# Kernel optimization log

Hardware: AMD Instinct MI355X
Metric: run time of the kernel (lower is better)

## Reference

```python
import jax, jax.numpy as jnp
import numpy as np

B, T, D, A = 32, 4096, 512, 64


def setup_inputs() -> dict:
    key = jax.random.key(0)
    k_x, k_m, k_w1, k_b1, k_w2 = jax.random.split(key, 5)
    x = jax.random.normal(k_x, (B, T, D), dtype=jnp.float32)
    mask = jax.random.randint(k_m, (B, T), 0, 2) > 0
    mask = mask.at[:, 0].set(True)  # guarantee >=1 valid step per row
    # params of attention MLP: Linear(D->A) with bias, Linear(A->1) no bias
    W1 = jax.random.normal(k_w1, (A, D), dtype=jnp.float32) / np.sqrt(D)
    b1 = jax.random.normal(k_b1, (A,), dtype=jnp.float32) * 0.01
    w2 = jax.random.normal(k_w2, (A,), dtype=jnp.float32) / np.sqrt(A)
    return {"x": x, "mask": mask, "W1": W1, "b1": b1, "w2": w2}


def reference(x, mask, W1, b1, w2):
    h = jnp.tanh(jnp.einsum('btd,ad->bta', x, W1) + b1)
    scores = jnp.einsum('bta,a->bt', h, w2)
    scores = jnp.where(mask, scores, -jnp.inf)
    weights = jax.nn.softmax(scores, axis=-1)          # (B, T)
    context = jnp.einsum('bt,btd->bd', weights, x)     # (B, D)
    return context, weights
```

## Files before the change

### kernel.cpp

```cpp
#include <hip/hip_runtime.h>
#include <math.h>

#define NB 32
#define NT 4096
#define ND 512
#define NA 64
#define ND4 (ND / 4)
#define RPB 128
#define NBLK (NB * NT / RPB)
#define NPW (NT / RPB)

typedef __attribute__((ext_vector_type(8))) short short8;
typedef __attribute__((ext_vector_type(4))) float f32x4;

__device__ __forceinline__ uint cvtpk(float f0, float f1) {
    uint r;
    asm("v_cvt_pk_bf16_f32 %0, %1, %2" : "=v"(r) : "v"(f0), "v"(f1));
    return r;
}
__device__ __forceinline__ void split2(float f0, float f1, uint& hw, uint& lw) {
    hw = cvtpk(f0, f1);
    float r0 = f0 - __uint_as_float(hw << 16);
    float r1 = f1 - __uint_as_float(hw & 0xffff0000u);
    lw = cvtpk(r0, r1);
}
__device__ __forceinline__ void split8(float4 a, float4 b, short8& hi, short8& lo) {
    union U { short8 s; uint u[4]; } H, L;
    split2(a.x, a.y, H.u[0], L.u[0]);
    split2(a.z, a.w, H.u[1], L.u[1]);
    split2(b.x, b.y, H.u[2], L.u[2]);
    split2(b.z, b.w, H.u[3], L.u[3]);
    hi = H.s; lo = L.s;
}

__device__ __forceinline__ float fast_tanh(float z) {
    z = fminf(fmaxf(z, -15.f), 15.f);
    float t = __expf(2.f * z);
    return (t - 1.f) * __builtin_amdgcn_rcpf(t + 1.f);
}

__global__ __launch_bounds__(256) void k_prep(
    const float* __restrict__ W1, short8* __restrict__ whi, short8* __restrict__ wlo)
{
    int t = blockIdx.x * 256 + threadIdx.x;
    int l  = t & 63;
    int nt = (t >> 6) & 3;
    int ks = t >> 8;
    int a  = nt * 16 + (l & 15);
    int kb = ks * 32 + (l >> 4) * 8;
    const float* p = W1 + a * ND + kb;
    float4 u = *(const float4*)p;
    float4 v = *(const float4*)(p + 4);
    short8 hi, lo;
    split8(u, v, hi, lo);
    whi[t] = hi;
    wlo[t] = lo;
}

__global__ __launch_bounds__(256, 4) void k_fused(
    const float* __restrict__ x, const int* __restrict__ mask,
    const short8* __restrict__ whi, const short8* __restrict__ wlo,
    const float* __restrict__ b1, const float* __restrict__ w2,
    float* __restrict__ scores, float* __restrict__ pctx, float* __restrict__ pml)
{
    __shared__ float ctxl[4][ND];
    __shared__ float wmx[4], wlx[4];

    const int tid = threadIdx.x;
    const int wv  = tid >> 6;
    const int l   = tid & 63;
    const int lr  = l & 15;
    const int lq  = l >> 4;
    const size_t row0 = (size_t)blockIdx.x * RPB + (size_t)wv * 32;

    const float4* __restrict__ x4 = reinterpret_cast<const float4*>(x);
    const float* xb = x + (row0 + lr) * ND + lq * 8;

    float w2v[4], b1v[4];
#pragma unroll
    for (int nt = 0; nt < 4; ++nt) {
        w2v[nt] = w2[nt * 16 + lr];
        b1v[nt] = b1[nt * 16 + lr];
    }

    f32x4 acc[2][4];
#pragma unroll
    for (int mt = 0; mt < 2; ++mt)
#pragma unroll
        for (int nt = 0; nt < 4; ++nt) acc[mt][nt] = (f32x4)0.f;

    for (int ks = 0; ks < 16; ++ks) {
        short8 ahi[2], alo[2];
#pragma unroll
        for (int mt = 0; mt < 2; ++mt) {
            const float* p = xb + mt * 16 * ND + ks * 32;
            float4 u = *(const float4*)p;
            float4 v = *(const float4*)(p + 4);
            split8(u, v, ahi[mt], alo[mt]);
        }
#pragma unroll
        for (int nt = 0; nt < 4; ++nt) {
            short8 bh = whi[(ks * 4 + nt) * 64 + l];
            short8 bl = wlo[(ks * 4 + nt) * 64 + l];
#pragma unroll
            for (int mt = 0; mt < 2; ++mt) {
                acc[mt][nt] = __builtin_amdgcn_mfma_f32_16x16x32_bf16(ahi[mt], bh, acc[mt][nt], 0, 0, 0);
                acc[mt][nt] = __builtin_amdgcn_mfma_f32_16x16x32_bf16(ahi[mt], bl, acc[mt][nt], 0, 0, 0);
                acc[mt][nt] = __builtin_amdgcn_mfma_f32_16x16x32_bf16(alo[mt], bh, acc[mt][nt], 0, 0, 0);
            }
        }
    }

    float sval[2][4];
#pragma unroll
    for (int mt = 0; mt < 2; ++mt) {
#pragma unroll
        for (int rg = 0; rg < 4; ++rg) {
            float s = 0.f;
#pragma unroll
            for (int nt = 0; nt < 4; ++nt)
                s += w2v[nt] * fast_tanh(acc[mt][nt][rg] + b1v[nt]);
            s += __shfl_xor(s, 1);
            s += __shfl_xor(s, 2);
            s += __shfl_xor(s, 4);
            s += __shfl_xor(s, 8);
            int ridx = mt * 16 + lq * 4 + rg;
            bool valid = (mask[row0 + ridx] != 0);
            float sm = valid ? s : -INFINITY;
            if (lr == 0) scores[row0 + ridx] = sm;
            sval[mt][rg] = sm;
        }
    }

    float wm = -INFINITY;
#pragma unroll
    for (int mt = 0; mt < 2; ++mt)
#pragma unroll
        for (int rg = 0; rg < 4; ++rg) wm = fmaxf(wm, sval[mt][rg]);
    wm = fmaxf(wm, __shfl_xor(wm, 16));
    wm = fmaxf(wm, __shfl_xor(wm, 32));
    float wm_eff = (wm == -INFINITY) ? 0.f : wm;
    float ev[2][4];
#pragma unroll
    for (int mt = 0; mt < 2; ++mt)
#pragma unroll
        for (int rg = 0; rg < 4; ++rg) ev[mt][rg] = __expf(sval[mt][rg] - wm_eff);
    float wl = (ev[0][0] + ev[0][1]) + (ev[0][2] + ev[0][3])
             + (ev[1][0] + ev[1][1]) + (ev[1][2] + ev[1][3]);
    wl += __shfl_xor(wl, 16);
    wl += __shfl_xor(wl, 32);
    if (l == 0) { wmx[wv] = wm; wlx[wv] = wl; }

    float4 ca = {0.f, 0.f, 0.f, 0.f}, cb = {0.f, 0.f, 0.f, 0.f};
#pragma unroll
    for (int t = 0; t < 32; ++t) {
        float e = __shfl(ev[t >> 4][t & 3], ((t >> 2) & 3) * 16);
        float4 xa = x4[(row0 + t) * ND4 + l];
        float4 xv = x4[(row0 + t) * ND4 + 64 + l];
        ca.x = fmaf(e, xa.x, ca.x);
        ca.y = fmaf(e, xa.y, ca.y);
        ca.z = fmaf(e, xa.z, ca.z);
        ca.w = fmaf(e, xa.w, ca.w);
        cb.x = fmaf(e, xv.x, cb.x);
        cb.y = fmaf(e, xv.y, cb.y);
        cb.z = fmaf(e, xv.z, cb.z);
        cb.w = fmaf(e, xv.w, cb.w);
    }

    __syncthreads();
    float mb = fmaxf(fmaxf(wmx[0], wmx[1]), fmaxf(wmx[2], wmx[3]));
    float mb_eff = (mb == -INFINITY) ? 0.f : mb;
    float sw = __expf(wm - mb_eff);
    float4 sa = {ca.x * sw, ca.y * sw, ca.z * sw, ca.w * sw};
    float4 sb = {cb.x * sw, cb.y * sw, cb.z * sw, cb.w * sw};
    *(float4*)&ctxl[wv][4 * l]       = sa;
    *(float4*)&ctxl[wv][256 + 4 * l] = sb;
    __syncthreads();

    float s0 = (ctxl[0][tid] + ctxl[1][tid]) + (ctxl[2][tid] + ctxl[3][tid]);
    int t2 = tid + 256;
    float s1 = (ctxl[0][t2] + ctxl[1][t2]) + (ctxl[2][t2] + ctxl[3][t2]);
    pctx[(size_t)blockIdx.x * ND + tid] = s0;
    pctx[(size_t)blockIdx.x * ND + t2]  = s1;
    if (tid == 0) {
        float lt = wlx[0] * __expf(wmx[0] - mb_eff) + wlx[1] * __expf(wmx[1] - mb_eff)
                 + wlx[2] * __expf(wmx[2] - mb_eff) + wlx[3] * __expf(wmx[3] - mb_eff);
        pml[blockIdx.x * 2]     = mb;
        pml[blockIdx.x * 2 + 1] = lt;
    }
}

__global__ __launch_bounds__(256) void k_merge(
    const float* __restrict__ pctx, const float* __restrict__ pml,
    float* __restrict__ ctx, float* __restrict__ mbden)
{
    int b = blockIdx.x, tid = threadIdx.x;
    float m_b = -INFINITY;
    for (int i = 0; i < NPW; ++i) m_b = fmaxf(m_b, pml[(b * NPW + i) * 2]);
    float denom = 0.f;
    for (int i = 0; i < NPW; ++i) {
        float mi = pml[(b * NPW + i) * 2];
        float li = pml[(b * NPW + i) * 2 + 1];
        denom += li * expf(mi - m_b);
    }
    float inv = 1.f / denom;
    int d0 = 2 * tid;
    float a0 = 0.f, a1 = 0.f;
    for (int i = 0; i < NPW; ++i) {
        float s = expf(pml[(b * NPW + i) * 2] - m_b);
        a0 = fmaf(pctx[(size_t)(b * NPW + i) * ND + d0],     s, a0);
        a1 = fmaf(pctx[(size_t)(b * NPW + i) * ND + d0 + 1], s, a1);
    }
    ctx[(size_t)b * ND + d0]     = a0 * inv;
    ctx[(size_t)b * ND + d0 + 1] = a1 * inv;
    if (tid == 0) {
        mbden[b * 2]     = m_b;
        mbden[b * 2 + 1] = denom;
    }
}

__global__ __launch_bounds__(256) void k_weights(
    const float* __restrict__ scores, const float* __restrict__ mbden,
    float* __restrict__ weights)
{
    int i = blockIdx.x * 256 + threadIdx.x;
    int b = i >> 12;
    float m  = mbden[b * 2];
    float dn = mbden[b * 2 + 1];
    weights[i] = expf(scores[i] - m) / dn;
}

extern "C" void kernel_launch(void* const* d_in, const int* in_sizes, int n_in,
                              void* d_out, int out_size, void* d_ws, size_t ws_size,
                              hipStream_t stream)
{
    const float* x    = (const float*)d_in[0];
    const int*   mask = (const int*)d_in[1];
    const float* W1   = (const float*)d_in[2];
    const float* b1   = (const float*)d_in[3];
    const float* w2   = (const float*)d_in[4];

    float* ctx     = (float*)d_out;
    float* weights = (float*)d_out + NB * ND;

    float* ws      = (float*)d_ws;
    float* scores  = ws;
    float* pctx    = ws + NB * NT;
    float* pml     = pctx + (size_t)NBLK * ND;
    float* mbden   = pml + NBLK * 2;
    short8* whi    = (short8*)(mbden + NB * 2);
    short8* wlo    = whi + 16 * 4 * 64;

    k_prep<<<16, 256, 0, stream>>>(W1, whi, wlo);
    k_fused<<<NBLK, 256, 0, stream>>>(x, mask, whi, wlo, b1, w2,
                                      scores, pctx, pml);
    k_merge<<<NB, 256, 0, stream>>>(pctx, pml, ctx, mbden);
    k_weights<<<NB * NT / 256, 256, 0, stream>>>(scores, mbden, weights);
}
```

Baseline: 110.0 us.

## Drop softmax max-subtraction and accumulate context using raw exponentiated scores

Drops the running-max stabilisation from the softmax. The tanh-bounded scores are exponentiated directly, so per-block partial contexts and denominators can be plain sums. This removes the per-wave max reduction, the rescale exps and the max bookkeeping in the merge and weights kernels. The weights kernel becomes a single multiply by a precomputed inverse denominator. It also interleaves the context accumulation into each 16-row score tile. The risk is exp overflow or lost precision if sum|w2| were large, since correctness now relies on scores being bounded by the w2 magnitude.

Result: slower. 206.4 us (+87.6%).

```diff
diff --git a/kernel.cpp b/kernel.cpp
--- a/kernel.cpp
+++ b/kernel.cpp
@@ -61,10 +61,10 @@
     const float* __restrict__ x, const int* __restrict__ mask,
     const short8* __restrict__ whi, const short8* __restrict__ wlo,
     const float* __restrict__ b1, const float* __restrict__ w2,
-    float* __restrict__ scores, float* __restrict__ pctx, float* __restrict__ pml)
+    float* __restrict__ escore, float* __restrict__ pctx, float* __restrict__ pden)
 {
     __shared__ float ctxl[4][ND];
-    __shared__ float wmx[4], wlx[4];
+    __shared__ float wlx[4];
 
     const int tid = threadIdx.x;
     const int wv  = tid >> 6;
@@ -111,7 +111,8 @@
         }
     }
 
-    float sval[2][4];
+    float ev[2][4];
+    float4 ca = {0.f, 0.f, 0.f, 0.f}, cb = {0.f, 0.f, 0.f, 0.f};
 #pragma unroll
     for (int mt = 0; mt < 2; ++mt) {
 #pragma unroll
@@ -126,55 +127,35 @@
             s += __shfl_xor(s, 8);
             int ridx = mt * 16 + lq * 4 + rg;
             bool valid = (mask[row0 + ridx] != 0);
-            float sm = valid ? s : -INFINITY;
-            if (lr == 0) scores[row0 + ridx] = sm;
-            sval[mt][rg] = sm;
-        }
-    }
-
-    float wm = -INFINITY;
-#pragma unroll
-    for (int mt = 0; mt < 2; ++mt)
-#pragma unroll
-        for (int rg = 0; rg < 4; ++rg) wm = fmaxf(wm, sval[mt][rg]);
-    wm = fmaxf(wm, __shfl_xor(wm, 16));
-    wm = fmaxf(wm, __shfl_xor(wm, 32));
-    float wm_eff = (wm == -INFINITY) ? 0.f : wm;
-    float ev[2][4];
-#pragma unroll
-    for (int mt = 0; mt < 2; ++mt)
-#pragma unroll
-        for (int rg = 0; rg < 4; ++rg) ev[mt][rg] = __expf(sval[mt][rg] - wm_eff);
+            float e = valid ? __expf(s) : 0.f;
+            if (lr == 0) escore[row0 + ridx] = e;
+            ev[mt][rg] = e;
+        }
+#pragma unroll
+        for (int t = 0; t < 16; ++t) {
+            float e = __shfl(ev[mt][t & 3], ((t >> 2) & 3) * 16);
+            size_t r = row0 + mt * 16 + t;
+            float4 xa = x4[r * ND4 + l];
+            float4 xv = x4[r * ND4 + 64 + l];
+            ca.x = fmaf(e, xa.x, ca.x);
+            ca.y = fmaf(e, xa.y, ca.y);
+            ca.z = fmaf(e, xa.z, ca.z);
+            ca.w = fmaf(e, xa.w, ca.w);
+            cb.x = fmaf(e, xv.x, cb.x);
+            cb.y = fmaf(e, xv.y, cb.y);
+            cb.z = fmaf(e, xv.z, cb.z);
+            cb.w = fmaf(e, xv.w, cb.w);
+        }
+    }
+
     float wl = (ev[0][0] + ev[0][1]) + (ev[0][2] + ev[0][3])
              + (ev[1][0] + ev[1][1]) + (ev[1][2] + ev[1][3]);
     wl += __shfl_xor(wl, 16);
     wl += __shfl_xor(wl, 32);
-    if (l == 0) { wmx[wv] = wm; wlx[wv] = wl; }
-
-    float4 ca = {0.f, 0.f, 0.f, 0.f}, cb = {0.f, 0.f, 0.f, 0.f};
-#pragma unroll
-    for (int t = 0; t < 32; ++t) {
-        float e = __shfl(ev[t >> 4][t & 3], ((t >> 2) & 3) * 16);
-        float4 xa = x4[(row0 + t) * ND4 + l];
-        float4 xv = x4[(row0 + t) * ND4 + 64 + l];
-        ca.x = fmaf(e, xa.x, ca.x);
-        ca.y = fmaf(e, xa.y, ca.y);
-        ca.z = fmaf(e, xa.z, ca.z);
-        ca.w = fmaf(e, xa.w, ca.w);
-        cb.x = fmaf(e, xv.x, cb.x);
-        cb.y = fmaf(e, xv.y, cb.y);
-        cb.z = fmaf(e, xv.z, cb.z);
-        cb.w = fmaf(e, xv.w, cb.w);
-    }
-
-    __syncthreads();
-    float mb = fmaxf(fmaxf(wmx[0], wmx[1]), fmaxf(wmx[2], wmx[3]));
-    float mb_eff = (mb == -INFINITY) ? 0.f : mb;
-    float sw = __expf(wm - mb_eff);
-    float4 sa = {ca.x * sw, ca.y * sw, ca.z * sw, ca.w * sw};
-    float4 sb = {cb.x * sw, cb.y * sw, cb.z * sw, cb.w * sw};
-    *(float4*)&ctxl[wv][4 * l]       = sa;
-    *(float4*)&ctxl[wv][256 + 4 * l] = sb;
+    if (l == 0) wlx[wv] = wl;
+
+    *(float4*)&ctxl[wv][4 * l]       = ca;
+    *(float4*)&ctxl[wv][256 + 4 * l] = cb;
     __syncthreads();
 
     float s0 = (ctxl[0][tid] + ctxl[1][tid]) + (ctxl[2][tid] + ctxl[3][tid]);
@@ -182,52 +163,36 @@
     float s1 = (ctxl[0][t2] + ctxl[1][t2]) + (ctxl[2][t2] + ctxl[3][t2]);
     pctx[(size_t)blockIdx.x * ND + tid] = s0;
     pctx[(size_t)blockIdx.x * ND + t2]  = s1;
-    if (tid == 0) {
-        float lt = wlx[0] * __expf(wmx[0] - mb_eff) + wlx[1] * __expf(wmx[1] - mb_eff)
-                 + wlx[2] * __expf(wmx[2] - mb_eff) + wlx[3] * __expf(wmx[3] - mb_eff);
-        pml[blockIdx.x * 2]     = mb;
-        pml[blockIdx.x * 2 + 1] = lt;
-    }
+    if (tid == 0)
+        pden[blockIdx.x] = (wlx[0] + wlx[1]) + (wlx[2] + wlx[3]);
 }
 
 __global__ __launch_bounds__(256) void k_merge(
-    const float* __restrict__ pctx, const float* __restrict__ pml,
-    float* __restrict__ ctx, float* __restrict__ mbden)
+    const float* __restrict__ pctx, const float* __restrict__ pden,
+    float* __restrict__ ctx, float* __restrict__ invden)
 {
     int b = blockIdx.x, tid = threadIdx.x;
-    float m_b = -INFINITY;
-    for (int i = 0; i < NPW; ++i) m_b = fmaxf(m_b, pml[(b * NPW + i) * 2]);
     float denom = 0.f;
-    for (int i = 0; i < NPW; ++i) {
-        float mi = pml[(b * NPW + i) * 2];
-        float li = pml[(b * NPW + i) * 2 + 1];
-        denom += li * expf(mi - m_b);
-    }
+    for (int i = 0; i < NPW; ++i) denom += pden[b * NPW + i];
     float inv = 1.f / denom;
     int d0 = 2 * tid;
     float a0 = 0.f, a1 = 0.f;
     for (int i = 0; i < NPW; ++i) {
-        float s = expf(pml[(b * NPW + i) * 2] - m_b);
-        a0 = fmaf(pctx[(size_t)(b * NPW + i) * ND + d0],     s, a0);
-        a1 = fmaf(pctx[(size_t)(b * NPW + i) * ND + d0 + 1], s, a1);
+        a0 += pctx[(size_t)(b * NPW + i) * ND + d0];
+        a1 += pctx[(size_t)(b * NPW + i) * ND + d0 + 1];
     }
     ctx[(size_t)b * ND + d0]     = a0 * inv;
     ctx[(size_t)b * ND + d0 + 1] = a1 * inv;
-    if (tid == 0) {
-        mbden[b * 2]     = m_b;
-        mbden[b * 2 + 1] = denom;
-    }
+    if (tid == 0) invden[b] = inv;
 }
 
 __global__ __launch_bounds__(256) void k_weights(
-    const float* __restrict__ scores, const float* __restrict__ mbden,
+    const float* __restrict__ escore, const float* __restrict__ invden,
     float* __restrict__ weights)
 {
     int i = blockIdx.x * 256 + threadIdx.x;
     int b = i >> 12;
-    float m  = mbden[b * 2];
-    float dn = mbden[b * 2 + 1];
-    weights[i] = expf(scores[i] - m) / dn;
+    weights[i] = escore[i] * invden[b];
 }
 
 extern "C" void kernel_launch(void* const* d_in, const int* in_sizes, int n_in,
@@ -244,16 +209,16 @@
     float* weights = (float*)d_out + NB * ND;
 
     float* ws      = (float*)d_ws;
-    float* scores  = ws;
+    float* escore  = ws;
     float* pctx    = ws + NB * NT;
-    float* pml     = pctx + (size_t)NBLK * ND;
-    float* mbden   = pml + NBLK * 2;
-    short8* whi    = (short8*)(mbden + NB * 2);
+    float* pden    = pctx + (size_t)NBLK * ND;
+    float* invden  = pden + NBLK;
+    short8* whi    = (short8*)(invden + NB);
     short8* wlo    = whi + 16 * 4 * 64;
 
     k_prep<<<16, 256, 0, stream>>>(W1, whi, wlo);
     k_fused<<<NBLK, 256, 0, stream>>>(x, mask, whi, wlo, b1, w2,
-                                      scores, pctx, pml);
-    k_merge<<<NB, 256, 0, stream>>>(pctx, pml, ctx, mbden);
-    k_weights<<<NB * NT / 256, 256, 0, stream>>>(scores, mbden, weights);
-}
+                                      escore, pctx, pden);
+    k_merge<<<NB, 256, 0, stream>>>(pctx, pden, ctx, invden);
+    k_weights<<<NB * NT / 256, 256, 0, stream>>>(escore, invden, weights);
+}
```
